# Kernel tuning notes

Hardware: AMD Instinct MI355X
Metric: run time of the kernel (lower is better)

## Reference

```python
import jax, jax.numpy as jnp
import numpy as np

R = 16
ALPHA = 16.0
SCALE = ALPHA / max(1, R)  # alpha / max(1, r)


def setup_inputs() -> dict:
    key = jax.random.key(0)
    k1, k2, k3, k4, k5 = jax.random.split(key, 5)
    B, S, D_IN, D_OUT = 4, 4096, 4096, 4096
    x = jax.random.normal(k1, (B, S, D_IN), dtype=jnp.float32)
    weight = jax.random.normal(k2, (D_OUT, D_IN), dtype=jnp.float32) * (1.0 / np.sqrt(D_IN))
    bias = jax.random.normal(k3, (D_OUT,), dtype=jnp.float32)
    lora_A = jax.random.normal(k4, (R, D_IN), dtype=jnp.float32) * (1.0 / np.sqrt(D_IN))
    lora_B = jax.random.normal(k5, (D_OUT, R), dtype=jnp.float32) * (1.0 / np.sqrt(R))
    return {"x": x, "weight": weight, "bias": bias, "lora_A": lora_A, "lora_B": lora_B}


def reference(x, weight, bias, lora_A, lora_B):
    # base = F.linear(x, weight, bias) = x @ W^T + b
    base = jnp.einsum('bsi,oi->bso', x, weight) + bias
    # lora = x @ (B @ A)^T = (x @ A^T) @ B^T  (chained low-rank, same math)
    xa = jnp.einsum('bsi,ri->bsr', x, lora_A)   # [B,S,r]
    lora = jnp.einsum('bsr,or->bso', xa, lora_B)  # [B,S,out]
    return base + SCALE * lora
```

## Files before the change

kernel.cpp:

```cpp
#include <hip/hip_runtime.h>
#include <stdint.h>

#define M_DIM 16384
#define N_DIM 4096
#define K_DIM 4096
#define LORA_SCALE 1.0f

#define BM 256
#define BN 256
#define BK 64
#define NT (K_DIM / BK)

typedef _Float16 half8 __attribute__((ext_vector_type(8)));
typedef float f32x4 __attribute__((ext_vector_type(4)));

__global__ __launch_bounds__(256) void prep_kernel(const float* __restrict__ x,
                                                   _Float16* __restrict__ xb,
                                                   const float* __restrict__ W,
                                                   const float* __restrict__ lA,
                                                   const float* __restrict__ lB,
                                                   _Float16* __restrict__ wp) {
    __shared__ float A_lds[16][256];
    __shared__ float B_lds[256];
    const int t = threadIdx.x;

    if (blockIdx.x < 256) {
        const int n0 = blockIdx.x * 16;
        B_lds[t] = lB[(size_t)n0 * 16 + t];
        for (int kc = 0; kc < 16; ++kc) {
            const int k = kc * 256 + t;
            __syncthreads();
#pragma unroll
            for (int r = 0; r < 16; ++r) A_lds[r][t] = lA[(size_t)r * K_DIM + k];
            __syncthreads();
#pragma unroll 4
            for (int row = 0; row < 16; ++row) {
                float acc = W[(size_t)(n0 + row) * K_DIM + k];
                float dot = 0.f;
#pragma unroll
                for (int r = 0; r < 16; ++r) dot += B_lds[row * 16 + r] * A_lds[r][t];
                acc += LORA_SCALE * dot;
                wp[(size_t)(n0 + row) * K_DIM + k] = (_Float16)acc;
            }
        }
        return;
    }

    const size_t base = ((size_t)(blockIdx.x - 256) * 256 + t) * 8;
    f32x4 a = *(const f32x4*)(x + base);
    f32x4 b = *(const f32x4*)(x + base + 4);
    half8 h;
    h[0] = (_Float16)a[0]; h[1] = (_Float16)a[1];
    h[2] = (_Float16)a[2]; h[3] = (_Float16)a[3];
    h[4] = (_Float16)b[0]; h[5] = (_Float16)b[1];
    h[6] = (_Float16)b[2]; h[7] = (_Float16)b[3];
    *(half8*)(xb + base) = h;
}

__device__ __forceinline__ void load_lds16(const void* g, void* l) {
    __builtin_amdgcn_global_load_lds(
        (const __attribute__((address_space(1))) unsigned int*)(uintptr_t)g,
        (__attribute__((address_space(3))) unsigned int*)(uintptr_t)l,
        16, 0, 0);
}

__global__ __launch_bounds__(512, 2) void gemm256_kernel(const _Float16* __restrict__ A,
                                                         const _Float16* __restrict__ B,
                                                         const float* __restrict__ bias,
                                                         float* __restrict__ C) {
    __shared__ _Float16 As[2][2][256 * 32];
    __shared__ _Float16 Bs[2][2][256 * 32];

    const int tid  = threadIdx.x;
    const int lane = tid & 63;
    const int wave = tid >> 6;
    const int wm   = wave >> 2;
    const int wn   = wave & 3;
    const int quad = lane >> 4;
    const int r16  = lane & 15;
    const int swz  = (quad ^ ((r16 >> 1) & 3)) << 3;

    const int bid = blockIdx.x;
    const int id  = (bid & 7) * 128 + (bid >> 3);
    const int m0  = (id >> 4) * BM;
    const int n0  = (id & 15) * BN;

    const int  srow = tid >> 2;
    const int  scol = (((tid & 3) ^ ((tid >> 3) & 3)) << 3);
    const _Float16* gA = A + (size_t)(m0 + srow) * K_DIM + scol;
    const _Float16* gB = B + (size_t)(n0 + srow) * K_DIM + scol;
    const int ldst0 = tid * 8;
    const int ldst1 = (tid + 512) * 8;

    const int arow = (wm * 128 + r16) * 32 + swz;
    const int brow = (wn * 64 + r16) * 32 + swz;

    f32x4 acc[8][4] = {};
    half8 a[8], b0, b1;

#define ISSUE_A(DB, KH, T) do { \
        const _Float16* g_ = gA + (size_t)((T) * 64 + (KH) * 32); \
        load_lds16(g_, &As[DB][KH][ldst0]); \
        load_lds16(g_ + (size_t)128 * K_DIM, &As[DB][KH][ldst1]); \
    } while (0)
#define ISSUE_B(DB, KH, T) do { \
        const _Float16* g_ = gB + (size_t)((T) * 64 + (KH) * 32); \
        load_lds16(g_, &Bs[DB][KH][ldst0]); \
        load_lds16(g_ + (size_t)128 * K_DIM, &Bs[DB][KH][ldst1]); \
    } while (0)

#define MID() do { \
        asm volatile("" ::: "memory"); __builtin_amdgcn_sched_barrier(0); \
        __builtin_amdgcn_s_barrier(); \
        asm volatile("s_waitcnt lgkmcnt(0)" ::: "memory"); \
        __builtin_amdgcn_sched_barrier(0); \
        __builtin_amdgcn_s_setprio(1); \
    } while (0)
#define ENDP() do { \
        __builtin_amdgcn_s_setprio(0); \
        asm volatile("" ::: "memory"); __builtin_amdgcn_sched_barrier(0); \
        __builtin_amdgcn_s_barrier(); \
    } while (0)

#define MFMA16(JLO) \
        _Pragma("unroll") \
        for (int i_ = 0; i_ < 8; ++i_) { \
            acc[i_][JLO]       = __builtin_amdgcn_mfma_f32_16x16x32_f16(a[i_], b0, acc[i_][JLO], 0, 0, 0); \
            acc[i_][(JLO) + 1] = __builtin_amdgcn_mfma_f32_16x16x32_f16(a[i_], b1, acc[i_][(JLO) + 1], 0, 0, 0); \
        }

#define PH_A(DB, KH, JLO, ISS) do { \
        _Pragma("unroll") \
        for (int i_ = 0; i_ < 8; ++i_) a[i_] = *(const half8*)&As[DB][KH][arow + i_ * 512]; \
        b0 = *(const half8*)&Bs[DB][KH][brow + (JLO) * 512]; \
        b1 = *(const half8*)&Bs[DB][KH][brow + ((JLO) + 1) * 512]; \
        ISS; MID(); MFMA16(JLO) ENDP(); \
    } while (0)
#define PH_B(DB, KH, JLO, ISS) do { \
        b0 = *(const half8*)&Bs[DB][KH][brow + (JLO) * 512]; \
        b1 = *(const half8*)&Bs[DB][KH][brow + ((JLO) + 1) * 512]; \
        ISS; MID(); MFMA16(JLO) ENDP(); \
    } while (0)
#define PH_B3(DB, KH, JLO, ISS) do { \
        b0 = *(const half8*)&Bs[DB][KH][brow + (JLO) * 512]; \
        b1 = *(const half8*)&Bs[DB][KH][brow + ((JLO) + 1) * 512]; \
        ISS; MID(); MFMA16(JLO) \
    } while (0)

#define TILE(DB, T1, T2) do { \
        PH_A(DB, 0, 0, ISSUE_B(1 - (DB), 1, T1)); \
        PH_B(DB, 0, 2, ISSUE_A(DB, 0, T2)); \
        PH_A(DB, 1, 0, ISSUE_B(DB, 0, T2)); \
        PH_B3(DB, 1, 2, ISSUE_A(DB, 1, T2)); \
    } while (0)
#define ENDT6() do { \
        __builtin_amdgcn_s_setprio(0); \
        asm volatile("" ::: "memory"); __builtin_amdgcn_sched_barrier(0); \
        asm volatile("s_waitcnt vmcnt(6)" ::: "memory"); \
        __builtin_amdgcn_s_barrier(); \
    } while (0)

    ISSUE_A(0, 0, 0); ISSUE_B(0, 0, 0); ISSUE_A(0, 1, 0); ISSUE_B(0, 1, 0);
    ISSUE_A(1, 0, 1); ISSUE_B(1, 0, 1); ISSUE_A(1, 1, 1);
    asm volatile("s_waitcnt vmcnt(6)" ::: "memory");
    __builtin_amdgcn_s_barrier();

#pragma unroll 1
    for (int ip = 0; ip < 31; ++ip) {
        const int t1 = 2 * ip + 1, t2 = 2 * ip + 2, t3 = 2 * ip + 3;
        TILE(0, t1, t2);
        ENDT6();
        TILE(1, t2, t3);
        ENDT6();
    }
    PH_A(0, 0, 0, ISSUE_B(1, 1, 63));
    PH_B(0, 0, 2, (void)0);
    PH_A(0, 1, 0, (void)0);
    PH_B3(0, 1, 2, (void)0);
    __builtin_amdgcn_s_setprio(0);
    asm volatile("" ::: "memory"); __builtin_amdgcn_sched_barrier(0);
    asm volatile("s_waitcnt vmcnt(0)" ::: "memory");
    __builtin_amdgcn_s_barrier();
    PH_A(1, 0, 0, (void)0);
    PH_B(1, 0, 2, (void)0);
    PH_A(1, 1, 0, (void)0);
    PH_B3(1, 1, 2, (void)0);
    __builtin_amdgcn_s_setprio(0);

#undef TILE
#undef ENDT6
#undef PH_A
#undef PH_B
#undef PH_B3
#undef MFMA16
#undef MID
#undef ENDP
#undef ISSUE_A
#undef ISSUE_B

#pragma unroll
    for (int j = 0; j < 4; ++j) {
        const int n = n0 + wn * 64 + j * 16 + r16;
        const float bv = bias[n];
#pragma unroll
        for (int i = 0; i < 8; ++i) {
            const int mbase = m0 + wm * 128 + i * 16 + quad * 4;
#pragma unroll
            for (int r = 0; r < 4; ++r) {
                C[(size_t)(mbase + r) * N_DIM + n] = acc[i][j][r] + bv;
            }
        }
    }
}

extern "C" void kernel_launch(void* const* d_in, const int* in_sizes, int n_in,
                              void* d_out, int out_size, void* d_ws, size_t ws_size,
                              hipStream_t stream) {
    const float* x      = (const float*)d_in[0];
    const float* weight = (const float*)d_in[1];
    const float* bias   = (const float*)d_in[2];
    const float* lora_A = (const float*)d_in[3];
    const float* lora_B = (const float*)d_in[4];
    float* out = (float*)d_out;

    _Float16* xb = (_Float16*)d_ws;
    _Float16* wp = (_Float16*)((char*)d_ws + (size_t)M_DIM * K_DIM * 2);

    prep_kernel<<<dim3(256 + (M_DIM * (size_t)K_DIM) / (256 * 8)), dim3(256), 0, stream>>>(
        x, xb, weight, lora_A, lora_B, wp);
    gemm256_kernel<<<dim3((M_DIM / BM) * (N_DIM / BN)), dim3(512), 0, stream>>>(xb, wp, bias, out);
}
```

Measured before the change: 941.7 us.

## Vectorize weight-merge prep and reorder GEMM phases to cut A-fragment register pressure

The weight+LoRA merge prep is rewritten so each thread processes 8 contiguous weight elements with vector loads, spread across many more blocks instead of 256 blocks looping over K. This removes the LDS staging and syncs and lowers the prep kernel's tail latency. The GEMM inner phase is restructured to hold 4 A and 4 B fragments (half the previous A registers) and to split work by M halves rather than N halves. The global-to-LDS issue order is rearranged to match, which changes register pressure and load/compute overlap.

```diff
diff --git a/kernel.cpp b/kernel.cpp
--- a/kernel.cpp
+++ b/kernel.cpp
@@ -20,33 +20,41 @@
                                                    const float* __restrict__ lA,
                                                    const float* __restrict__ lB,
                                                    _Float16* __restrict__ wp) {
-    __shared__ float A_lds[16][256];
-    __shared__ float B_lds[256];
     const int t = threadIdx.x;
-
-    if (blockIdx.x < 256) {
-        const int n0 = blockIdx.x * 16;
-        B_lds[t] = lB[(size_t)n0 * 16 + t];
-        for (int kc = 0; kc < 16; ++kc) {
-            const int k = kc * 256 + t;
-            __syncthreads();
-#pragma unroll
-            for (int r = 0; r < 16; ++r) A_lds[r][t] = lA[(size_t)r * K_DIM + k];
-            __syncthreads();
-#pragma unroll 4
-            for (int row = 0; row < 16; ++row) {
-                float acc = W[(size_t)(n0 + row) * K_DIM + k];
-                float dot = 0.f;
-#pragma unroll
-                for (int r = 0; r < 16; ++r) dot += B_lds[row * 16 + r] * A_lds[r][t];
-                acc += LORA_SCALE * dot;
-                wp[(size_t)(n0 + row) * K_DIM + k] = (_Float16)acc;
-            }
+    const int WBLK = (N_DIM * K_DIM) / (256 * 8);
+
+    if (blockIdx.x < WBLK) {
+        const size_t base = ((size_t)blockIdx.x * 256 + t) * 8;
+        const int n = (int)(base >> 12);
+        const int k = (int)(base & (K_DIM - 1));
+        const int ns = __builtin_amdgcn_readfirstlane(n);
+        float Brow[16];
+#pragma unroll
+        for (int r = 0; r < 16; ++r) Brow[r] = lB[(size_t)ns * 16 + r];
+
+        f32x4 w0 = *(const f32x4*)(W + base);
+        f32x4 w1 = *(const f32x4*)(W + base + 4);
+        f32x4 d0 = {0.f, 0.f, 0.f, 0.f}, d1 = {0.f, 0.f, 0.f, 0.f};
+#pragma unroll
+        for (int r = 0; r < 16; ++r) {
+            const float* ar = lA + (size_t)r * K_DIM + k;
+            f32x4 a0 = *(const f32x4*)ar;
+            f32x4 a1 = *(const f32x4*)(ar + 4);
+            d0 += Brow[r] * a0;
+            d1 += Brow[r] * a1;
         }
+        w0 += LORA_SCALE * d0;
+        w1 += LORA_SCALE * d1;
+        half8 h;
+        h[0] = (_Float16)w0[0]; h[1] = (_Float16)w0[1];
+        h[2] = (_Float16)w0[2]; h[3] = (_Float16)w0[3];
+        h[4] = (_Float16)w1[0]; h[5] = (_Float16)w1[1];
+        h[6] = (_Float16)w1[2]; h[7] = (_Float16)w1[3];
+        *(half8*)(wp + base) = h;
         return;
     }
 
-    const size_t base = ((size_t)(blockIdx.x - 256) * 256 + t) * 8;
+    const size_t base = ((size_t)(blockIdx.x - WBLK) * 256 + t) * 8;
     f32x4 a = *(const f32x4*)(x + base);
     f32x4 b = *(const f32x4*)(x + base + 4);
     half8 h;
@@ -96,7 +104,7 @@
     const int brow = (wn * 64 + r16) * 32 + swz;
 
     f32x4 acc[8][4] = {};
-    half8 a[8], b0, b1;
+    half8 a[4], b[4];
 
 #define ISSUE_A(DB, KH, T) do { \
         const _Float16* g_ = gA + (size_t)((T) * 64 + (KH) * 32); \
@@ -122,36 +130,37 @@
         __builtin_amdgcn_s_barrier(); \
     } while (0)
 
-#define MFMA16(JLO) \
-        _Pragma("unroll") \
-        for (int i_ = 0; i_ < 8; ++i_) { \
-            acc[i_][JLO]       = __builtin_amdgcn_mfma_f32_16x16x32_f16(a[i_], b0, acc[i_][JLO], 0, 0, 0); \
-            acc[i_][(JLO) + 1] = __builtin_amdgcn_mfma_f32_16x16x32_f16(a[i_], b1, acc[i_][(JLO) + 1], 0, 0, 0); \
-        }
-
-#define PH_A(DB, KH, JLO, ISS) do { \
-        _Pragma("unroll") \
-        for (int i_ = 0; i_ < 8; ++i_) a[i_] = *(const half8*)&As[DB][KH][arow + i_ * 512]; \
-        b0 = *(const half8*)&Bs[DB][KH][brow + (JLO) * 512]; \
-        b1 = *(const half8*)&Bs[DB][KH][brow + ((JLO) + 1) * 512]; \
-        ISS; MID(); MFMA16(JLO) ENDP(); \
-    } while (0)
-#define PH_B(DB, KH, JLO, ISS) do { \
-        b0 = *(const half8*)&Bs[DB][KH][brow + (JLO) * 512]; \
-        b1 = *(const half8*)&Bs[DB][KH][brow + ((JLO) + 1) * 512]; \
-        ISS; MID(); MFMA16(JLO) ENDP(); \
-    } while (0)
-#define PH_B3(DB, KH, JLO, ISS) do { \
-        b0 = *(const half8*)&Bs[DB][KH][brow + (JLO) * 512]; \
-        b1 = *(const half8*)&Bs[DB][KH][brow + ((JLO) + 1) * 512]; \
-        ISS; MID(); MFMA16(JLO) \
+#define MFMA16(MLO) \
+        _Pragma("unroll") \
+        for (int i_ = 0; i_ < 4; ++i_) \
+            _Pragma("unroll") \
+            for (int j_ = 0; j_ < 4; ++j_) \
+                acc[(MLO) + i_][j_] = __builtin_amdgcn_mfma_f32_16x16x32_f16( \
+                    a[i_], b[j_], acc[(MLO) + i_][j_], 0, 0, 0);
+
+#define PH_BA(DB, KH, ISS) do { \
+        _Pragma("unroll") \
+        for (int j_ = 0; j_ < 4; ++j_) b[j_] = *(const half8*)&Bs[DB][KH][brow + j_ * 512]; \
+        _Pragma("unroll") \
+        for (int i_ = 0; i_ < 4; ++i_) a[i_] = *(const half8*)&As[DB][KH][arow + i_ * 512]; \
+        ISS; MID(); MFMA16(0) ENDP(); \
+    } while (0)
+#define PH_A2(DB, KH, ISS) do { \
+        _Pragma("unroll") \
+        for (int i_ = 0; i_ < 4; ++i_) a[i_] = *(const half8*)&As[DB][KH][arow + (i_ + 4) * 512]; \
+        ISS; MID(); MFMA16(4) ENDP(); \
+    } while (0)
+#define PH_A2L(DB, KH, ISS) do { \
+        _Pragma("unroll") \
+        for (int i_ = 0; i_ < 4; ++i_) a[i_] = *(const half8*)&As[DB][KH][arow + (i_ + 4) * 512]; \
+        ISS; MID(); MFMA16(4) \
     } while (0)
 
 #define TILE(DB, T1, T2) do { \
-        PH_A(DB, 0, 0, ISSUE_B(1 - (DB), 1, T1)); \
-        PH_B(DB, 0, 2, ISSUE_A(DB, 0, T2)); \
-        PH_A(DB, 1, 0, ISSUE_B(DB, 0, T2)); \
-        PH_B3(DB, 1, 2, ISSUE_A(DB, 1, T2)); \
+        PH_BA(DB, 0, ISSUE_A(1 - (DB), 1, T1)); \
+        PH_A2(DB, 0, ISSUE_B(DB, 0, T2)); \
+        PH_BA(DB, 1, ISSUE_A(DB, 0, T2)); \
+        PH_A2L(DB, 1, ISSUE_B(DB, 1, T2)); \
     } while (0)
 #define ENDT6() do { \
         __builtin_amdgcn_s_setprio(0); \
@@ -160,8 +169,8 @@
         __builtin_amdgcn_s_barrier(); \
     } while (0)
 
-    ISSUE_A(0, 0, 0); ISSUE_B(0, 0, 0); ISSUE_A(0, 1, 0); ISSUE_B(0, 1, 0);
-    ISSUE_A(1, 0, 1); ISSUE_B(1, 0, 1); ISSUE_A(1, 1, 1);
+    ISSUE_B(0, 0, 0); ISSUE_A(0, 0, 0); ISSUE_B(0, 1, 0); ISSUE_A(0, 1, 0);
+    ISSUE_B(1, 0, 1); ISSUE_A(1, 0, 1); ISSUE_B(1, 1, 1);
     asm volatile("s_waitcnt vmcnt(6)" ::: "memory");
     __builtin_amdgcn_s_barrier();
 
@@ -173,25 +182,25 @@
         TILE(1, t2, t3);
         ENDT6();
     }
-    PH_A(0, 0, 0, ISSUE_B(1, 1, 63));
-    PH_B(0, 0, 2, (void)0);
-    PH_A(0, 1, 0, (void)0);
-    PH_B3(0, 1, 2, (void)0);
+    PH_BA(0, 0, ISSUE_A(1, 1, 63));
+    PH_A2(0, 0, (void)0);
+    PH_BA(0, 1, (void)0);
+    PH_A2L(0, 1, (void)0);
     __builtin_amdgcn_s_setprio(0);
     asm volatile("" ::: "memory"); __builtin_amdgcn_sched_barrier(0);
     asm volatile("s_waitcnt vmcnt(0)" ::: "memory");
     __builtin_amdgcn_s_barrier();
-    PH_A(1, 0, 0, (void)0);
-    PH_B(1, 0, 2, (void)0);
-    PH_A(1, 1, 0, (void)0);
-    PH_B3(1, 1, 2, (void)0);
+    PH_BA(1, 0, (void)0);
+    PH_A2(1, 0, (void)0);
+    PH_BA(1, 1, (void)0);
+    PH_A2L(1, 1, (void)0);
     __builtin_amdgcn_s_setprio(0);
 
 #undef TILE
 #undef ENDT6
-#undef PH_A
-#undef PH_B
-#undef PH_B3
+#undef PH_BA
+#undef PH_A2
+#undef PH_A2L
 #undef MFMA16
 #undef MID
 #undef ENDP
@@ -226,7 +235,8 @@
     _Float16* xb = (_Float16*)d_ws;
     _Float16* wp = (_Float16*)((char*)d_ws + (size_t)M_DIM * K_DIM * 2);
 
-    prep_kernel<<<dim3(256 + (M_DIM * (size_t)K_DIM) / (256 * 8)), dim3(256), 0, stream>>>(
-        x, xb, weight, lora_A, lora_B, wp);
+    const int wblk = (N_DIM * K_DIM) / (256 * 8);
+    const int xblk = (int)((M_DIM * (size_t)K_DIM) / (256 * 8));
+    prep_kernel<<<dim3(wblk + xblk), dim3(256), 0, stream>>>(x, xb, weight, lora_A, lora_B, wp);
     gemm256_kernel<<<dim3((M_DIM / BM) * (N_DIM / BN)), dim3(512), 0, stream>>>(xb, wp, bias, out);
 }
```

Measured after the change: 989.5 us. 1.05x slower.
